# Optimization experiments

Hardware: AMD Instinct MI355X
Metric: run time of the kernel (lower is better)

The kernel has to match this reference:

```python
import jax, jax.numpy as jnp
import numpy as np

B, N, C = 4, 48 * 64, 256
H, W = 48, 64


def _positional_encodings(batch, dtype=jnp.float32):
    # (x^2, y^2, xy, x, y, 1) encoding; matches get_positional_encodings with intrinsics=None
    ys = jnp.linspace(-1.0, 1.0, H, dtype=dtype)
    xs = jnp.linspace(-1.0, 1.0, W, dtype=dtype)
    p3 = jnp.tile(ys, W)            # [N] : ys repeated W times (torch .repeat(B, w))
    p4 = jnp.repeat(xs, H)          # [N] : each x repeated H times (repeat_interleave)
    pos = jnp.stack([p3 * p3, p4 * p4, p3 * p4, p3, p4, jnp.ones_like(p3)], axis=-1)  # [N,6]
    return jnp.broadcast_to(pos, (batch, N, 6))


def setup_inputs() -> dict:
    key = jax.random.key(0)
    k1, k2, k3, k4 = jax.random.split(key, 4)
    x1 = jax.random.normal(k1, (B, N, C), dtype=jnp.float32)
    x2 = jax.random.normal(k2, (B, N, C), dtype=jnp.float32)
    corr = jax.random.normal(k3, (B, 1, H, W, H, W), dtype=jnp.float32)
    W_proj = jax.random.normal(k4, (C + 6, C), dtype=jnp.float32) * (1.0 / np.sqrt(C + 6))
    b_proj = jnp.zeros((C,), dtype=jnp.float32)
    return {"x1": x1, "x2": x2, "corr": corr, "W_proj": W_proj, "b_proj": b_proj}


def reference(x1, x2, corr, W_proj, b_proj):
    b, n, c = x1.shape
    a = corr.reshape(b, n, n)                      # squeeze(1) + double flatten
    # dual softmax (row-wise * column-wise)
    s_row = jax.nn.softmax(a, axis=-1)
    s_col = jax.nn.softmax(a, axis=-2)
    attn_f1 = s_row * s_col                        # [B,N,N]
    attn_f2 = jnp.swapaxes(attn_f1, -2, -1)        # softmax(a^T,-1)*softmax(a^T,-2) == attn_f1^T

    pos = _positional_encodings(b, dtype=x1.dtype)
    v1 = jnp.concatenate([x1, pos], axis=2)        # [B,N,C+6]
    v2 = jnp.concatenate([x2, pos], axis=2)

    # bilinear products v^T @ attn @ v  -> [B, C+6, C+6]
    fund1 = jnp.einsum('bnc,bnm,bmd->bcd', v1, attn_f1, v1)
    fund2 = jnp.einsum('bnc,bnm,bmd->bcd', v2, attn_f2, v2)

    fund1 = jnp.swapaxes(fund1, -2, -1)
    fund2 = jnp.swapaxes(fund2, -2, -1)

    out1 = fund1 @ W_proj + b_proj                 # proj_fundamental
    out2 = fund2 @ W_proj + b_proj
    return (out2, out1)                            # (fundamental_2, fundamental_1)
```

## Files before the change

### kernel.cpp

```cpp
#include <hip/hip_runtime.h>
#include <math.h>

#define NB 4
#define NN 3072
#define NC 256
#define CP 262
#define KG 384
#define XW 528
#define MD 272
#define K3S 8
#define HH 48
#define WW 64
#define LOG2E 1.4426950408889634f

typedef short short8 __attribute__((ext_vector_type(8)));
typedef short short4v __attribute__((ext_vector_type(4)));
typedef float f32x4 __attribute__((ext_vector_type(4)));
typedef unsigned int uint4v __attribute__((ext_vector_type(4)));

__device__ __forceinline__ float fexp2(float x) {
#if __has_builtin(__builtin_amdgcn_exp2f)
    return __builtin_amdgcn_exp2f(x);
#else
    return __exp2f(x);
#endif
}

__device__ __forceinline__ void bsplit(float v, short& h, short& l) {
    unsigned u = __float_as_uint(v);
    h = (short)(u >> 16);
    float r = v - __uint_as_float(u & 0xFFFF0000u);
    l = (short)(__float_as_uint(r) >> 16);
}

__device__ __forceinline__ void fma4(float4& c, float a, float4 b) {
    c.x = fmaf(a, b.x, c.x);
    c.y = fmaf(a, b.y, c.y);
    c.z = fmaf(a, b.z, c.z);
    c.w = fmaf(a, b.w, c.w);
}

__global__ __launch_bounds__(256) void k_prep(const float* __restrict__ x1,
                                              const float* __restrict__ x2,
                                              short* __restrict__ Xh, short* __restrict__ Xl) {
    int id = blockIdx.x * 256 + threadIdx.x;
    if (id >= NB * KG * XW) return;
    int col = id % XW;
    int rest = id / XW;
    int kg = rest % KG;
    int b = rest / KG;
    short* ph = Xh + (size_t)id * 8;
    short* pl = Xl + (size_t)id * 8;
    if (col < 512) {
        const float* src = (col < 256 ? x1 : x2) + ((size_t)b * NN + kg * 8) * NC + (col & 255);
#pragma unroll
        for (int j = 0; j < 8; j++) {
            short hs, ls;
            bsplit(src[(size_t)j * NC], hs, ls);
            ph[j] = hs; pl[j] = ls;
        }
    } else {
        int c = col - 512;
#pragma unroll
        for (int j = 0; j < 8; j++) {
            int k = kg * 8 + j;
            int ip4 = k / HH;
            int ip3 = k - ip4 * HH;
            float p3 = -1.f + 2.f * (float)ip3 / 47.f;
            float p4 = -1.f + 2.f * (float)ip4 / 63.f;
            float v = 0.f;
            if (c == 0) v = p3 * p3;
            else if (c == 1) v = p4 * p4;
            else if (c == 2) v = p3 * p4;
            else if (c == 3) v = p3;
            else if (c == 4) v = p4;
            else if (c == 5) v = 1.f;
            short hs, ls;
            bsplit(v, hs, ls);
            ph[j] = hs; pl[j] = ls;
        }
    }
}

__global__ __launch_bounds__(256) void k_stats(const float* __restrict__ corr,
                                               float* __restrict__ pM, float* __restrict__ pS,
                                               float* __restrict__ rmS, float* __restrict__ irs) {
    int bid = blockIdx.x;
    int t = threadIdx.x;
    __shared__ float red[8];
    if (bid < 384) {
        int cx = bid % 12;
        int b = (bid / 12) & 3;
        int ch = bid / 48;
        int m = cx * 256 + t;
        const float* p = corr + (size_t)b * NN * NN + (size_t)ch * 384 * NN + m;
        float mx[4], s[4];
#pragma unroll
        for (int i = 0; i < 4; i++) { mx[i] = -3.4e38f; s[i] = 0.f; }
        for (int r = 0; r < 384; r += 4) {
#pragma unroll
            for (int i = 0; i < 4; i++) {
                float x = p[(size_t)(r + i) * NN];
                float mn = fmaxf(mx[i], x);
                s[i] = s[i] * __expf(mx[i] - mn) + __expf(x - mn);
                mx[i] = mn;
            }
        }
        float mn01 = fmaxf(mx[0], mx[1]);
        float s01 = s[0] * __expf(mx[0] - mn01) + s[1] * __expf(mx[1] - mn01);
        float mn23 = fmaxf(mx[2], mx[3]);
        float s23 = s[2] * __expf(mx[2] - mn23) + s[3] * __expf(mx[3] - mn23);
        float mnA = fmaxf(mn01, mn23);
        float sA = s01 * __expf(mn01 - mnA) + s23 * __expf(mn23 - mnA);
        pM[((size_t)ch * NB + b) * NN + m] = mnA;
        pS[((size_t)ch * NB + b) * NN + m] = sA;
    } else {
        int rid = bid - 384;
        int b = rid / NN;
        int n = rid - b * NN;
        const float4* p = (const float4*)(corr + ((size_t)b * NN + n) * NN);
        float4 v[3];
        float m = -3.4e38f;
#pragma unroll
        for (int i = 0; i < 3; i++) {
            v[i] = p[t + i * 256];
            m = fmaxf(m, fmaxf(fmaxf(v[i].x, v[i].y), fmaxf(v[i].z, v[i].w)));
        }
#pragma unroll
        for (int off = 32; off; off >>= 1) m = fmaxf(m, __shfl_xor(m, off));
        if ((t & 63) == 0) red[t >> 6] = m;
        __syncthreads();
        m = fmaxf(fmaxf(red[0], red[1]), fmaxf(red[2], red[3]));
        float s = 0.f;
#pragma unroll
        for (int i = 0; i < 3; i++)
            s += __expf(v[i].x - m) + __expf(v[i].y - m) + __expf(v[i].z - m) + __expf(v[i].w - m);
#pragma unroll
        for (int off = 32; off; off >>= 1) s += __shfl_xor(s, off);
        if ((t & 63) == 0) red[4 + (t >> 6)] = s;
        __syncthreads();
        if (t == 0) {
            float st = red[4] + red[5] + red[6] + red[7];
            rmS[b * NN + n] = m * LOG2E;
            irs[b * NN + n] = 1.f / st;
        }
    }
}

__global__ __launch_bounds__(256) void k_colcombine(const float* __restrict__ pM,
                                                    const float* __restrict__ pS,
                                                    float* __restrict__ ccS) {
    int idx = blockIdx.x * 256 + threadIdx.x;
    if (idx >= NB * NN) return;
    float mx = -3.4e38f, s = 0.f;
#pragma unroll
    for (int ch = 0; ch < 8; ch++) {
        float m2 = pM[(size_t)ch * NB * NN + idx];
        float s2 = pS[(size_t)ch * NB * NN + idx];
        float mn = fmaxf(mx, m2);
        s = s * __expf(mx - mn) + s2 * __expf(m2 - mn);
        mx = mn;
    }
    ccS[idx] = (mx + logf(s)) * LOG2E;
}

#define MFMA_CLUSTER(AHF, ALF, BHF, BLF)                                                          \
    {                                                                                             \
        _Pragma("unroll") for (int fr_ = 0; fr_ < 3; fr_++)                                       \
        _Pragma("unroll") for (int i_ = 0; i_ < 4; i_++)                                          \
            acc[fr_][i_] = __builtin_amdgcn_mfma_f32_16x16x32_bf16(AHF[fr_], BHF[i_], acc[fr_][i_], 0, 0, 0); \
        _Pragma("unroll") for (int fr_ = 0; fr_ < 3; fr_++)                                       \
        _Pragma("unroll") for (int i_ = 0; i_ < 4; i_++)                                          \
            acc[fr_][i_] = __builtin_amdgcn_mfma_f32_16x16x32_bf16(AHF[fr_], BLF[i_], acc[fr_][i_], 0, 0, 0); \
        _Pragma("unroll") for (int fr_ = 0; fr_ < 3; fr_++)                                       \
        _Pragma("unroll") for (int i_ = 0; i_ < 4; i_++)                                          \
            acc[fr_][i_] = __builtin_amdgcn_mfma_f32_16x16x32_bf16(ALF[fr_], BHF[i_], acc[fr_][i_], 0, 0, 0); \
    }

#define POS_CLUSTER(AHF, ALF, PBH, PBL)                                                           \
    {                                                                                             \
        _Pragma("unroll") for (int fr_ = 0; fr_ < 3; fr_++) {                                     \
            accP[fr_] = __builtin_amdgcn_mfma_f32_16x16x32_bf16(AHF[fr_], (PBH), accP[fr_], 0, 0, 0); \
            accP[fr_] = __builtin_amdgcn_mfma_f32_16x16x32_bf16(AHF[fr_], (PBL), accP[fr_], 0, 0, 0); \
            accP[fr_] = __builtin_amdgcn_mfma_f32_16x16x32_bf16(ALF[fr_], (PBH), accP[fr_], 0, 0, 0); \
        }                                                                                         \
    }

#define READ_AFRAGS(BUFH, BUFL, UNIT, AHF, ALF)                                                   \
    {                                                                                             \
        _Pragma("unroll") for (int fr_ = 0; fr_ < 3; fr_++) {                                     \
            int rowr_ = rbase + fr_ * 16 + row16;                                                 \
            int uidx_ = rowr_ * 32 + (((UNIT) ^ (rowr_ & 7)) << 2);                               \
            AHF[fr_] = *(const short8*)&(BUFH)[uidx_];                                            \
            ALF[fr_] = *(const short8*)&(BUFL)[uidx_];                                            \
        }                                                                                         \
    }

#define LOAD_B(PH, PL, BHF, BLF)                                                                  \
    {                                                                                             \
        _Pragma("unroll") for (int i_ = 0; i_ < 4; i_++) {                                        \
            BHF[i_] = *(const short8*)((PH) + i_ * 128);                                          \
            BLF[i_] = *(const short8*)((PL) + i_ * 128);                                          \
        }                                                                                         \
    }

#define STAGE_A(DSTH, DSTL, PC)                                                                   \
    {                                                                                             \
        f32x4 ccv0 = *(const f32x4*)&ccsh[(PC) * 64 + g * 16];                                    \
        f32x4 ccv1 = *(const f32x4*)&ccsh[(PC) * 64 + g * 16 + 4];                                \
        f32x4 ccv2 = *(const f32x4*)&ccsh[(PC) * 64 + g * 16 + 8];                                \
        f32x4 ccv3 = *(const f32x4*)&ccsh[(PC) * 64 + g * 16 + 12];                               \
        float ev[16];                                                                             \
        _Pragma("unroll") for (int q_ = 0; q_ < 4; q_++) {                                        \
            ev[q_]      = fexp2(fmaf(C2, cr[0][q_], rmn) - ccv0[q_]);                             \
            ev[4 + q_]  = fexp2(fmaf(C2, cr[1][q_], rmn) - ccv1[q_]);                             \
            ev[8 + q_]  = fexp2(fmaf(C2, cr[2][q_], rmn) - ccv2[q_]);                             \
            ev[12 + q_] = fexp2(fmaf(C2, cr[3][q_], rmn) - ccv3[q_]);                             \
        }                                                                                         \
        uint4v hi0, hi1, lo0, lo1;                                                                \
        _Pragma("unroll") for (int q_ = 0; q_ < 4; q_++) {                                        \
            unsigned u0 = __float_as_uint(ev[2 * q_]);                                            \
            unsigned u1 = __float_as_uint(ev[2 * q_ + 1]);                                        \
            hi0[q_] = __builtin_amdgcn_perm(u1, u0, 0x07060302u);                                 \
            float r0_ = ev[2 * q_] - __uint_as_float(u0 & 0xffff0000u);                           \
            float r1_ = ev[2 * q_ + 1] - __uint_as_float(u1 & 0xffff0000u);                       \
            lo0[q_] = __builtin_amdgcn_perm(__float_as_uint(r1_), __float_as_uint(r0_), 0x07060302u); \
            unsigned v0 = __float_as_uint(ev[8 + 2 * q_]);                                        \
            unsigned v1 = __float_as_uint(ev[8 + 2 * q_ + 1]);                                    \
            hi1[q_] = __builtin_amdgcn_perm(v1, v0, 0x07060302u);                                 \
            float t0_ = ev[8 + 2 * q_] - __uint_as_float(v0 & 0xffff0000u);                       \
            float t1_ = ev[8 + 2 * q_ + 1] - __uint_as_float(v1 & 0xffff0000u);                   \
            lo1[q_] = __builtin_amdgcn_perm(__float_as_uint(t1_), __float_as_uint(t0_), 0x07060302u); \
        }                                                                                         \
        *(uint4v*)&(DSTH)[widx0] = hi0;                                                           \
        *(uint4v*)&(DSTH)[widx1] = hi1;                                                           \
        *(uint4v*)&(DSTL)[widx0] = lo0;                                                           \
        *(uint4v*)&(DSTL)[widx1] = lo1;                                                           \
    }

__global__ __launch_bounds__(512, 2) void k2_mfma(const float* __restrict__ corr,
        const short* __restrict__ Xh, const short* __restrict__ Xl,
        const float* __restrict__ rmS, const float* __restrict__ irs,
        const float* __restrict__ ccS,
        short* __restrict__ Zh, short* __restrict__ Zl) {
    __shared__ __align__(16) unsigned AHs[2][96 * 32];
    __shared__ __align__(16) unsigned ALs[2][96 * 32];
    __shared__ __align__(16) float ccsh[NN];

    const float C2 = 2.f * LOG2E;
    const size_t BSTEP = (size_t)4 * XW * 8;

    int bid = blockIdx.x;
    int xcd = bid & 7, sub = bid >> 3;
    int b = xcd >> 1;
    int which = sub & 1;
    int rowblk = (xcd & 1) + ((sub >> 1) << 1);
    int n0 = rowblk * 96;

    int t = threadIdx.x;
    int w = t >> 6, l = t & 63;
    int row16 = l & 15, slot = l >> 4;
    int rg = w & 1, cg = w >> 1;
    int rbase = rg * 48;
    bool posw = (which == 0) && (cg == 3);
    bool writer = (t < 384);
    int wrow = t >> 2, g = t & 3;
    int widx0 = wrow * 32 + (((2 * g) ^ (wrow & 7)) << 2);
    int widx1 = wrow * 32 + (((2 * g + 1) ^ (wrow & 7)) << 2);

    {
        const f32x4* src = (const f32x4*)(ccS + (size_t)b * NN);
        for (int i = t; i < NN / 4; i += 512) ((f32x4*)ccsh)[i] = src[i];
    }

    const float* corrR = corr;
    float rmn = 0.f;
    if (writer) {
        corrR = corr + ((size_t)b * NN + n0 + wrow) * NN + g * 16;
        rmn = -rmS[b * NN + n0 + wrow];
    }

    int col0 = which * 256 + cg * 64 + row16;
    const short* bh = Xh + ((size_t)(b * KG + slot) * XW + col0) * 8;
    const short* bl = Xl + ((size_t)(b * KG + slot) * XW + col0) * 8;
    const short* ph = Xh + ((size_t)(b * KG + slot) * XW + 512 + row16) * 8;
    const short* plp = Xl + ((size_t)(b * KG + slot) * XW + 512 + row16) * 8;

    f32x4 acc[3][4];
    f32x4 accP[3];
    const f32x4 zz = {0.f, 0.f, 0.f, 0.f};
#pragma unroll
    for (int fr = 0; fr < 3; fr++) {
#pragma unroll
        for (int i = 0; i < 4; i++) acc[fr][i] = zz;
        accP[fr] = zz;
    }

    short8 BhA[4], BlA[4], BhB[4], BlB[4];
    short8 PbhA = {0,0,0,0,0,0,0,0}, PblA = PbhA, PbhB = PbhA, PblB = PbhA;
    LOAD_B(bh, bl, BhA, BlA);
    if (posw) { PbhA = *(const short8*)ph; PblA = *(const short8*)plp; }

    f32x4 cr[4];
    __syncthreads();
    if (writer) {
#pragma unroll
        for (int q = 0; q < 4; q++) cr[q] = *(const f32x4*)(corrR + q * 4);
        STAGE_A(AHs[0], ALs[0], 0);
#pragma unroll
        for (int q = 0; q < 4; q++) cr[q] = *(const f32x4*)(corrR + 64 + q * 4);
    }
    asm volatile("s_waitcnt lgkmcnt(0)" ::: "memory");
    __builtin_amdgcn_s_barrier();

    int cur = 0;
    for (int p = 0; p < 48; ++p) {
        const unsigned* AHc = &AHs[cur][0];
        const unsigned* ALc = &ALs[cur][0];
        unsigned* AHn = &AHs[cur ^ 1][0];
        unsigned* ALn = &ALs[cur ^ 1][0];
        short8 Ah[3], Al[3];
        READ_AFRAGS(AHc, ALc, slot, Ah, Al);
        bh += BSTEP; bl += BSTEP;
        LOAD_B(bh, bl, BhB, BlB);
        if (posw) { ph += BSTEP; plp += BSTEP; PbhB = *(const short8*)ph; PblB = *(const short8*)plp; }
        MFMA_CLUSTER(Ah, Al, BhA, BlA);
        if (posw) POS_CLUSTER(Ah, Al, PbhA, PblA);
        READ_AFRAGS(AHc, ALc, 4 + slot, Ah, Al);
        if (p < 47) {
            bh += BSTEP; bl += BSTEP;
            LOAD_B(bh, bl, BhA, BlA);
            if (posw) { ph += BSTEP; plp += BSTEP; PbhA = *(const short8*)ph; PblA = *(const short8*)plp; }
        }
        if (writer) {
            int pc = (p + 1 < 48) ? p + 1 : 47;
            STAGE_A(AHn, ALn, pc);
            int pn = (p + 2 < 48) ? p + 2 : 47;
#pragma unroll
            for (int q = 0; q < 4; q++) cr[q] = *(const f32x4*)(corrR + pn * 64 + q * 4);
        }
        MFMA_CLUSTER(Ah, Al, BhB, BlB);
        if (posw) POS_CLUSTER(Ah, Al, PbhB, PblB);
        asm volatile("s_waitcnt lgkmcnt(0)" ::: "memory");
        __builtin_amdgcn_s_barrier();
        cur ^= 1;
    }

#pragma unroll
    for (int fr = 0; fr < 3; fr++) {
        f32x4 sv = *(const f32x4*)(irs + b * NN + n0 + rbase + fr * 16 + slot * 4);
        int kgz = rowblk * 12 + rg * 6 + fr * 2 + (slot >> 1);
        int jb = (slot & 1) << 2;
#pragma unroll
        for (int i = 0; i < 4; i++) {
            int colv = which * 256 + cg * 64 + i * 16 + row16;
            size_t off = ((size_t)(b * KG + kgz) * XW + colv) * 8 + jb;
            short4v zh, zl;
#pragma unroll
            for (int r = 0; r < 4; r++) {
                float vv = acc[fr][i][r] * sv[r];
                short hs, ls; bsplit(vv, hs, ls);
                zh[r] = hs; zl[r] = ls;
            }
            *(short4v*)(Zh + off) = zh;
            *(short4v*)(Zl + off) = zl;
        }
        if (posw && cg == 3 && rg == (w & 1)) {  }
        if (posw) {
            size_t off = ((size_t)(b * KG + kgz) * XW + 512 + row16) * 8 + jb;
            short4v zh, zl;
#pragma unroll
            for (int r = 0; r < 4; r++) {
                float vv = accP[fr][r] * sv[r];
                short hs, ls; bsplit(vv, hs, ls);
                zh[r] = hs; zl[r] = ls;
            }
            *(short4v*)(Zh + off) = zh;
            *(short4v*)(Zl + off) = zl;
        }
    }
}

__global__ __launch_bounds__(256) void k3_mfma(const short* __restrict__ Xh, const short* __restrict__ Xl,
                                               const short* __restrict__ Zh, const short* __restrict__ Zl,
                                               float* __restrict__ Mpart) {
    int tile = blockIdx.x;
    int rt = tile / 3, ct = tile % 3;
    int mb = blockIdx.y;
    int mat = mb >> 2, b = mb & 3;
    int split = blockIdx.z;

    const int O0[4] = {0, 6, 12, 17};
    int r0f = O0[rt], rNf = O0[rt + 1] - r0f;
    int c0f = O0[ct], cNf = O0[ct + 1] - c0f;

    int t = threadIdx.x;
    int w = t >> 6, l = t & 63;
    int row16 = l & 15, slot = l >> 4;
    int wr = w >> 1, wc = w & 1;
    int rh = (rNf + 1) >> 1;
    int rbeg = r0f + (wr ? rh : 0);
    int rcnt = wr ? (rNf - rh) : rh;
    int chh = (cNf + 1) >> 1;
    int cbeg = c0f + (wc ? chh : 0);
    int ccnt = wc ? (cNf - chh) : chh;

    const short *Ah_, *Al_, *Bh_, *Bl_;
    int abase, bbase;
    if (mat == 0) { Ah_ = Xh; Al_ = Xl; Bh_ = Zh; Bl_ = Zl; abase = 0; bbase = 0; }
    else          { Ah_ = Zh; Al_ = Zl; Bh_ = Xh; Bl_ = Xl; abase = 256; bbase = 256; }

    int acol[3], bcol[3];
#pragma unroll
    for (int i = 0; i < 3; i++) {
        int fa = rbeg + i;
        acol[i] = ((fa < 16) ? (abase + fa * 16) : 512) + row16;
        int fb = cbeg + i;
        bcol[i] = ((fb < 16) ? (bbase + fb * 16) : 512) + row16;
    }

    f32x4 acc[3][3];
    const f32x4 zz = {0.f, 0.f, 0.f, 0.f};
#pragma unroll
    for (int i = 0; i < 3; i++)
#pragma unroll
        for (int j = 0; j < 3; j++) acc[i][j] = zz;

    for (int it = 0; it < 12; it++) {
        int kg = split * 48 + it * 4 + slot;
        size_t base = (size_t)(b * KG + kg) * XW;
        short8 Ah[3], Al[3], Bhf[3], Blf[3];
#pragma unroll
        for (int i = 0; i < 3; i++) {
            if (i < rcnt) {
                Ah[i] = *(const short8*)(Ah_ + (base + acol[i]) * 8);
                Al[i] = *(const short8*)(Al_ + (base + acol[i]) * 8);
            }
            if (i < ccnt) {
                Bhf[i] = *(const short8*)(Bh_ + (base + bcol[i]) * 8);
                Blf[i] = *(const short8*)(Bl_ + (base + bcol[i]) * 8);
            }
        }
#pragma unroll
        for (int i = 0; i < 3; i++) {
            if (i < rcnt) {
#pragma unroll
                for (int j = 0; j < 3; j++) {
                    if (j < ccnt) {
                        acc[i][j] = __builtin_amdgcn_mfma_f32_16x16x32_bf16(Ah[i], Bhf[j], acc[i][j], 0, 0, 0);
                        acc[i][j] = __builtin_amdgcn_mfma_f32_16x16x32_bf16(Al[i], Bhf[j], acc[i][j], 0, 0, 0);
                        acc[i][j] = __builtin_amdgcn_mfma_f32_16x16x32_bf16(Ah[i], Blf[j], acc[i][j], 0, 0, 0);
                    }
                }
            }
        }
    }

    float* Mp = Mpart + (size_t)(mb * K3S + split) * (MD * MD);
#pragma unroll
    for (int i = 0; i < 3; i++) {
        if (i < rcnt) {
#pragma unroll
            for (int j = 0; j < 3; j++) {
                if (j < ccnt) {
                    int r = (rbeg + i) * 16 + slot * 4;
                    int c = (cbeg + j) * 16 + row16;
#pragma unroll
                    for (int q = 0; q < 4; q++)
                        Mp[(size_t)(r + q) * MD + c] = acc[i][j][q];
                }
            }
        }
    }
}

__global__ __launch_bounds__(256) void k_mcombine(const float* __restrict__ Mpart, float* __restrict__ M) {
    const int per = MD * MD;
    int f4 = blockIdx.x * 256 + threadIdx.x;
    if (f4 >= (8 * per) / 4) return;
    int e = f4 * 4;
    int mb = e / per;
    int off = e - mb * per;
    const float* src = Mpart + (size_t)mb * K3S * per + off;
    float4 s = make_float4(0.f, 0.f, 0.f, 0.f);
#pragma unroll
    for (int sp = 0; sp < K3S; sp++) {
        float4 v = *(const float4*)(src + (size_t)sp * per);
        s.x += v.x; s.y += v.y; s.z += v.z; s.w += v.w;
    }
    *(float4*)(M + (size_t)mb * per + off) = s;
}

__global__ __launch_bounds__(256) void k4_proj(const float* __restrict__ M, const float* __restrict__ Wp,
                                               const float* __restrict__ bp, float* __restrict__ out) {
    int i0 = blockIdx.x * 16;
    int b = blockIdx.y;
    int mat = blockIdx.z;
    const float* Mp = M + (size_t)(mat * 4 + b) * (MD * MD);
    int t = threadIdx.x;
    int jt = t & 63, it = t >> 6;
    int j = jt * 4;
    float4 a0 = make_float4(0.f, 0.f, 0.f, 0.f), a1 = a0, a2 = a0, a3 = a0;
#pragma unroll 2
    for (int k = 0; k < CP; k++) {
        float4 w = *(const float4*)(Wp + (size_t)k * NC + j);
        float4 g = *(const float4*)(Mp + (size_t)k * MD + i0 + it * 4);
        fma4(a0, g.x, w); fma4(a1, g.y, w); fma4(a2, g.z, w); fma4(a3, g.w, w);
    }
    float4 bb = *(const float4*)(bp + j);
    a0.x += bb.x; a0.y += bb.y; a0.z += bb.z; a0.w += bb.w;
    a1.x += bb.x; a1.y += bb.y; a1.z += bb.z; a1.w += bb.w;
    a2.x += bb.x; a2.y += bb.y; a2.z += bb.z; a2.w += bb.w;
    a3.x += bb.x; a3.y += bb.y; a3.z += bb.z; a3.w += bb.w;
    float* ob = out + (mat == 0 ? (size_t)NB * CP * NC : (size_t)0) + (size_t)b * CP * NC;
    int i = i0 + it * 4;
    if (i + 0 < CP) *(float4*)(ob + (size_t)(i + 0) * NC + j) = a0;
    if (i + 1 < CP) *(float4*)(ob + (size_t)(i + 1) * NC + j) = a1;
    if (i + 2 < CP) *(float4*)(ob + (size_t)(i + 2) * NC + j) = a2;
    if (i + 3 < CP) *(float4*)(ob + (size_t)(i + 3) * NC + j) = a3;
}

extern "C" void kernel_launch(void* const* d_in, const int* in_sizes, int n_in,
                              void* d_out, int out_size, void* d_ws, size_t ws_size,
                              hipStream_t stream) {
    const float* x1 = (const float*)d_in[0];
    const float* x2 = (const float*)d_in[1];
    const float* corr = (const float*)d_in[2];
    const float* Wp = (const float*)d_in[3];
    const float* bp = (const float*)d_in[4];
    float* out = (float*)d_out;
    float* w = (float*)d_ws;

    const size_t XSZ = (size_t)NB * KG * XW * 8;

    size_t o = 0;
    float* rmS = w + o;   o += NB * NN;
    float* irs = w + o;   o += NB * NN;
    float* ccS = w + o;   o += NB * NN;
    float* pM = w + o;    o += 8 * NB * NN;
    float* pS = w + o;    o += 8 * NB * NN;
    short* Xh = (short*)(w + o); o += XSZ / 2;
    short* Xl = (short*)(w + o); o += XSZ / 2;
    short* Zh = (short*)(w + o); o += XSZ / 2;
    short* Zl = (short*)(w + o); o += XSZ / 2;
    float* Mpart = w + o; o += (size_t)8 * K3S * MD * MD;
    float* M = w + o;     o += (size_t)8 * MD * MD;

    k_prep<<<dim3(3168), dim3(256), 0, stream>>>(x1, x2, Xh, Xl);
    k_stats<<<dim3(384 + NB * NN), dim3(256), 0, stream>>>(corr, pM, pS, rmS, irs);
    k_colcombine<<<dim3(48), dim3(256), 0, stream>>>(pM, pS, ccS);
    k2_mfma<<<dim3(256), dim3(512), 0, stream>>>(corr, Xh, Xl, rmS, irs, ccS, Zh, Zl);
    k3_mfma<<<dim3(9, 8, K3S), dim3(256), 0, stream>>>(Xh, Xl, Zh, Zl, Mpart);
    k_mcombine<<<dim3(578), dim3(256), 0, stream>>>(Mpart, M);
    k4_proj<<<dim3(17, NB, 2), dim3(256), 0, stream>>>(M, Wp, bp, out);
}
```

Measured before the change: 248.1 us.

## Fuse prep/colcombine/mcombine into neighbors and retile k2 warps over rows

Merges the bf16 split prep work into the stats kernel, moves the column-softmax combine into k2's prologue, and folds the K-split partial reduction into the projection kernel. This drops three launches and their intermediate buffers. Row stats now use one wave per row instead of a block-level reduction with barriers. In k2, each warp now covers all 96 rows and 32 columns, and the positional-encoding MFMA work rotates across warps with a shared-memory reduction at the end. The costs are redundant combine work per k2 block, eight-fold partial reads per k-step in the projection, and a larger A-fragment register footprint.

```diff
diff --git a/kernel.cpp b/kernel.cpp
--- a/kernel.cpp
+++ b/kernel.cpp
@@ -40,54 +40,14 @@
     c.w = fmaf(a, b.w, c.w);
 }
 
-__global__ __launch_bounds__(256) void k_prep(const float* __restrict__ x1,
-                                              const float* __restrict__ x2,
-                                              short* __restrict__ Xh, short* __restrict__ Xl) {
-    int id = blockIdx.x * 256 + threadIdx.x;
-    if (id >= NB * KG * XW) return;
-    int col = id % XW;
-    int rest = id / XW;
-    int kg = rest % KG;
-    int b = rest / KG;
-    short* ph = Xh + (size_t)id * 8;
-    short* pl = Xl + (size_t)id * 8;
-    if (col < 512) {
-        const float* src = (col < 256 ? x1 : x2) + ((size_t)b * NN + kg * 8) * NC + (col & 255);
-#pragma unroll
-        for (int j = 0; j < 8; j++) {
-            short hs, ls;
-            bsplit(src[(size_t)j * NC], hs, ls);
-            ph[j] = hs; pl[j] = ls;
-        }
-    } else {
-        int c = col - 512;
-#pragma unroll
-        for (int j = 0; j < 8; j++) {
-            int k = kg * 8 + j;
-            int ip4 = k / HH;
-            int ip3 = k - ip4 * HH;
-            float p3 = -1.f + 2.f * (float)ip3 / 47.f;
-            float p4 = -1.f + 2.f * (float)ip4 / 63.f;
-            float v = 0.f;
-            if (c == 0) v = p3 * p3;
-            else if (c == 1) v = p4 * p4;
-            else if (c == 2) v = p3 * p4;
-            else if (c == 3) v = p3;
-            else if (c == 4) v = p4;
-            else if (c == 5) v = 1.f;
-            short hs, ls;
-            bsplit(v, hs, ls);
-            ph[j] = hs; pl[j] = ls;
-        }
-    }
-}
-
 __global__ __launch_bounds__(256) void k_stats(const float* __restrict__ corr,
+                                               const float* __restrict__ x1,
+                                               const float* __restrict__ x2,
                                                float* __restrict__ pM, float* __restrict__ pS,
-                                               float* __restrict__ rmS, float* __restrict__ irs) {
+                                               float* __restrict__ rmS, float* __restrict__ irs,
+                                               short* __restrict__ Xh, short* __restrict__ Xl) {
     int bid = blockIdx.x;
     int t = threadIdx.x;
-    __shared__ float red[8];
     if (bid < 384) {
         int cx = bid % 12;
         int b = (bid / 12) & 3;
@@ -114,94 +74,120 @@
         float sA = s01 * __expf(mn01 - mnA) + s23 * __expf(mn23 - mnA);
         pM[((size_t)ch * NB + b) * NN + m] = mnA;
         pS[((size_t)ch * NB + b) * NN + m] = sA;
+    } else if (bid < 3456) {
+        int rid = bid - 384;
+        int b = rid / 768;
+        int r0 = (rid - b * 768) * 4;
+        int w = t >> 6, l = t & 63;
+        int n = r0 + w;
+        const float4* p = (const float4*)(corr + ((size_t)b * NN + n) * NN);
+        float4 v[12];
+        float m = -3.4e38f;
+#pragma unroll
+        for (int i = 0; i < 12; i++) {
+            v[i] = p[l + i * 64];
+            m = fmaxf(m, fmaxf(fmaxf(v[i].x, v[i].y), fmaxf(v[i].z, v[i].w)));
+        }
+#pragma unroll
+        for (int off = 1; off < 64; off <<= 1) m = fmaxf(m, __shfl_xor(m, off));
+        float s = 0.f;
+#pragma unroll
+        for (int i = 0; i < 12; i++)
+            s += __expf(v[i].x - m) + __expf(v[i].y - m) + __expf(v[i].z - m) + __expf(v[i].w - m);
+#pragma unroll
+        for (int off = 1; off < 64; off <<= 1) s += __shfl_xor(s, off);
+        if (l == 0) {
+            rmS[b * NN + n] = m * LOG2E;
+            irs[b * NN + n] = 1.f / s;
+        }
     } else {
-        int rid = bid - 384;
-        int b = rid / NN;
-        int n = rid - b * NN;
-        const float4* p = (const float4*)(corr + ((size_t)b * NN + n) * NN);
-        float4 v[3];
-        float m = -3.4e38f;
-#pragma unroll
-        for (int i = 0; i < 3; i++) {
-            v[i] = p[t + i * 256];
-            m = fmaxf(m, fmaxf(fmaxf(v[i].x, v[i].y), fmaxf(v[i].z, v[i].w)));
-        }
-#pragma unroll
-        for (int off = 32; off; off >>= 1) m = fmaxf(m, __shfl_xor(m, off));
-        if ((t & 63) == 0) red[t >> 6] = m;
-        __syncthreads();
-        m = fmaxf(fmaxf(red[0], red[1]), fmaxf(red[2], red[3]));
-        float s = 0.f;
-#pragma unroll
-        for (int i = 0; i < 3; i++)
-            s += __expf(v[i].x - m) + __expf(v[i].y - m) + __expf(v[i].z - m) + __expf(v[i].w - m);
-#pragma unroll
-        for (int off = 32; off; off >>= 1) s += __shfl_xor(s, off);
-        if ((t & 63) == 0) red[4 + (t >> 6)] = s;
-        __syncthreads();
-        if (t == 0) {
-            float st = red[4] + red[5] + red[6] + red[7];
-            rmS[b * NN + n] = m * LOG2E;
-            irs[b * NN + n] = 1.f / st;
-        }
-    }
-}
-
-__global__ __launch_bounds__(256) void k_colcombine(const float* __restrict__ pM,
-                                                    const float* __restrict__ pS,
-                                                    float* __restrict__ ccS) {
-    int idx = blockIdx.x * 256 + threadIdx.x;
-    if (idx >= NB * NN) return;
-    float mx = -3.4e38f, s = 0.f;
-#pragma unroll
-    for (int ch = 0; ch < 8; ch++) {
-        float m2 = pM[(size_t)ch * NB * NN + idx];
-        float s2 = pS[(size_t)ch * NB * NN + idx];
-        float mn = fmaxf(mx, m2);
-        s = s * __expf(mx - mn) + s2 * __expf(m2 - mn);
-        mx = mn;
-    }
-    ccS[idx] = (mx + logf(s)) * LOG2E;
-}
-
-#define MFMA_CLUSTER(AHF, ALF, BHF, BLF)                                                          \
-    {                                                                                             \
-        _Pragma("unroll") for (int fr_ = 0; fr_ < 3; fr_++)                                       \
-        _Pragma("unroll") for (int i_ = 0; i_ < 4; i_++)                                          \
+        int id = (bid - 3456) * 256 + t;
+        int col = id % XW;
+        int rest = id / XW;
+        int kg = rest % KG;
+        int b = rest / KG;
+        short* ph = Xh + (size_t)id * 8;
+        short* pl = Xl + (size_t)id * 8;
+        if (col < 512) {
+            const float* src = (col < 256 ? x1 : x2) + ((size_t)b * NN + kg * 8) * NC + (col & 255);
+#pragma unroll
+            for (int j = 0; j < 8; j++) {
+                short hs, ls;
+                bsplit(src[(size_t)j * NC], hs, ls);
+                ph[j] = hs; pl[j] = ls;
+            }
+        } else {
+            int c = col - 512;
+#pragma unroll
+            for (int j = 0; j < 8; j++) {
+                int k = kg * 8 + j;
+                int ip4 = k / HH;
+                int ip3 = k - ip4 * HH;
+                float p3 = -1.f + 2.f * (float)ip3 / 47.f;
+                float p4 = -1.f + 2.f * (float)ip4 / 63.f;
+                float v = 0.f;
+                if (c == 0) v = p3 * p3;
+                else if (c == 1) v = p4 * p4;
+                else if (c == 2) v = p3 * p4;
+                else if (c == 3) v = p3;
+                else if (c == 4) v = p4;
+                else if (c == 5) v = 1.f;
+                short hs, ls;
+                bsplit(v, hs, ls);
+                ph[j] = hs; pl[j] = ls;
+            }
+        }
+    }
+}
+
+struct SMemMain {
+    unsigned AH[2][96 * 32];
+    unsigned AL[2][96 * 32];
+    float ccsh[NN];
+};
+union SMemU {
+    SMemMain m;
+    float pdump[8 * 64 * 24];
+};
+
+#define LOAD_B2(PH, PL, BHF, BLF)                                           \
+    {                                                                        \
+        BHF[0] = *(const short8*)(PH);                                       \
+        BHF[1] = *(const short8*)((PH) + 128);                               \
+        BLF[0] = *(const short8*)(PL);                                       \
+        BLF[1] = *(const short8*)((PL) + 128);                               \
+    }
+
+#define READ_AFRAGS6(BUFH, BUFL, UNIT, AHF, ALF)                             \
+    {                                                                        \
+        _Pragma("unroll") for (int fr_ = 0; fr_ < 6; fr_++) {                \
+            int rowr_ = fr_ * 16 + row16;                                    \
+            int uidx_ = rowr_ * 32 + (((UNIT) ^ (rowr_ & 7)) << 2);          \
+            AHF[fr_] = *(const short8*)&(BUFH)[uidx_];                       \
+            ALF[fr_] = *(const short8*)&(BUFL)[uidx_];                       \
+        }                                                                    \
+    }
+
+#define MFMA_CLUSTER62(AHF, ALF, BHF, BLF)                                                         \
+    {                                                                                              \
+        _Pragma("unroll") for (int fr_ = 0; fr_ < 6; fr_++)                                        \
+        _Pragma("unroll") for (int i_ = 0; i_ < 2; i_++)                                           \
             acc[fr_][i_] = __builtin_amdgcn_mfma_f32_16x16x32_bf16(AHF[fr_], BHF[i_], acc[fr_][i_], 0, 0, 0); \
-        _Pragma("unroll") for (int fr_ = 0; fr_ < 3; fr_++)                                       \
-        _Pragma("unroll") for (int i_ = 0; i_ < 4; i_++)                                          \
+        _Pragma("unroll") for (int fr_ = 0; fr_ < 6; fr_++)                                        \
+        _Pragma("unroll") for (int i_ = 0; i_ < 2; i_++)                                           \
             acc[fr_][i_] = __builtin_amdgcn_mfma_f32_16x16x32_bf16(AHF[fr_], BLF[i_], acc[fr_][i_], 0, 0, 0); \
-        _Pragma("unroll") for (int fr_ = 0; fr_ < 3; fr_++)                                       \
-        _Pragma("unroll") for (int i_ = 0; i_ < 4; i_++)                                          \
+        _Pragma("unroll") for (int fr_ = 0; fr_ < 6; fr_++)                                        \
+        _Pragma("unroll") for (int i_ = 0; i_ < 2; i_++)                                           \
             acc[fr_][i_] = __builtin_amdgcn_mfma_f32_16x16x32_bf16(ALF[fr_], BHF[i_], acc[fr_][i_], 0, 0, 0); \
     }
 
-#define POS_CLUSTER(AHF, ALF, PBH, PBL)                                                           \
-    {                                                                                             \
-        _Pragma("unroll") for (int fr_ = 0; fr_ < 3; fr_++) {                                     \
+#define POS_CLUSTER6(AHF, ALF, PBH, PBL)                                                           \
+    {                                                                                              \
+        _Pragma("unroll") for (int fr_ = 0; fr_ < 6; fr_++) {                                      \
             accP[fr_] = __builtin_amdgcn_mfma_f32_16x16x32_bf16(AHF[fr_], (PBH), accP[fr_], 0, 0, 0); \
             accP[fr_] = __builtin_amdgcn_mfma_f32_16x16x32_bf16(AHF[fr_], (PBL), accP[fr_], 0, 0, 0); \
             accP[fr_] = __builtin_amdgcn_mfma_f32_16x16x32_bf16(ALF[fr_], (PBH), accP[fr_], 0, 0, 0); \
-        }                                                                                         \
-    }
-
-#define READ_AFRAGS(BUFH, BUFL, UNIT, AHF, ALF)                                                   \
-    {                                                                                             \
-        _Pragma("unroll") for (int fr_ = 0; fr_ < 3; fr_++) {                                     \
-            int rowr_ = rbase + fr_ * 16 + row16;                                                 \
-            int uidx_ = rowr_ * 32 + (((UNIT) ^ (rowr_ & 7)) << 2);                               \
-            AHF[fr_] = *(const short8*)&(BUFH)[uidx_];                                            \
-            ALF[fr_] = *(const short8*)&(BUFL)[uidx_];                                            \
-        }                                                                                         \
-    }
-
-#define LOAD_B(PH, PL, BHF, BLF)                                                                  \
-    {                                                                                             \
-        _Pragma("unroll") for (int i_ = 0; i_ < 4; i_++) {                                        \
-            BHF[i_] = *(const short8*)((PH) + i_ * 128);                                          \
-            BLF[i_] = *(const short8*)((PL) + i_ * 128);                                          \
-        }                                                                                         \
+        }                                                                                          \
     }
 
 #define STAGE_A(DSTH, DSTL, PC)                                                                   \
@@ -241,11 +227,10 @@
 __global__ __launch_bounds__(512, 2) void k2_mfma(const float* __restrict__ corr,
         const short* __restrict__ Xh, const short* __restrict__ Xl,
         const float* __restrict__ rmS, const float* __restrict__ irs,
-        const float* __restrict__ ccS,
+        const float* __restrict__ pM, const float* __restrict__ pS,
         short* __restrict__ Zh, short* __restrict__ Zl) {
-    __shared__ __align__(16) unsigned AHs[2][96 * 32];
-    __shared__ __align__(16) unsigned ALs[2][96 * 32];
-    __shared__ __align__(16) float ccsh[NN];
+    __shared__ SMemU sm;
+    float* ccsh = sm.m.ccsh;
 
     const float C2 = 2.f * LOG2E;
     const size_t BSTEP = (size_t)4 * XW * 8;
@@ -260,17 +245,23 @@
     int t = threadIdx.x;
     int w = t >> 6, l = t & 63;
     int row16 = l & 15, slot = l >> 4;
-    int rg = w & 1, cg = w >> 1;
-    int rbase = rg * 48;
-    bool posw = (which == 0) && (cg == 3);
+    bool doPos = (which == 0);
     bool writer = (t < 384);
     int wrow = t >> 2, g = t & 3;
     int widx0 = wrow * 32 + (((2 * g) ^ (wrow & 7)) << 2);
     int widx1 = wrow * 32 + (((2 * g + 1) ^ (wrow & 7)) << 2);
 
-    {
-        const f32x4* src = (const f32x4*)(ccS + (size_t)b * NN);
-        for (int i = t; i < NN / 4; i += 512) ((f32x4*)ccsh)[i] = src[i];
+    for (int c = t; c < NN; c += 512) {
+        float mx = -3.4e38f, s = 0.f;
+#pragma unroll
+        for (int ch = 0; ch < 8; ch++) {
+            float m2 = pM[(size_t)ch * NB * NN + b * NN + c];
+            float s2 = pS[(size_t)ch * NB * NN + b * NN + c];
+            float mn = fmaxf(mx, m2);
+            s = s * __expf(mx - mn) + s2 * __expf(m2 - mn);
+            mx = mn;
+        }
+        ccsh[c] = fmaf(mx, LOG2E, __log2f(s));
     }
 
     const float* corrR = corr;
@@ -280,33 +271,28 @@
         rmn = -rmS[b * NN + n0 + wrow];
     }
 
-    int col0 = which * 256 + cg * 64 + row16;
+    int col0 = which * 256 + w * 32 + row16;
     const short* bh = Xh + ((size_t)(b * KG + slot) * XW + col0) * 8;
     const short* bl = Xl + ((size_t)(b * KG + slot) * XW + col0) * 8;
-    const short* ph = Xh + ((size_t)(b * KG + slot) * XW + 512 + row16) * 8;
-    const short* plp = Xl + ((size_t)(b * KG + slot) * XW + 512 + row16) * 8;
-
-    f32x4 acc[3][4];
-    f32x4 accP[3];
+
+    f32x4 acc[6][2];
+    f32x4 accP[6];
     const f32x4 zz = {0.f, 0.f, 0.f, 0.f};
 #pragma unroll
-    for (int fr = 0; fr < 3; fr++) {
-#pragma unroll
-        for (int i = 0; i < 4; i++) acc[fr][i] = zz;
-        accP[fr] = zz;
-    }
-
-    short8 BhA[4], BlA[4], BhB[4], BlB[4];
-    short8 PbhA = {0,0,0,0,0,0,0,0}, PblA = PbhA, PbhB = PbhA, PblB = PbhA;
-    LOAD_B(bh, bl, BhA, BlA);
-    if (posw) { PbhA = *(const short8*)ph; PblA = *(const short8*)plp; }
+    for (int fr = 0; fr < 6; fr++) {
+        acc[fr][0] = zz; acc[fr][1] = zz; accP[fr] = zz;
+    }
+
+    short8 BhA[2], BlA[2], BhB[2], BlB[2];
+    short8 P0h = {0,0,0,0,0,0,0,0}, P0l = P0h, P1h = P0h, P1l = P0h;
+    LOAD_B2(bh, bl, BhA, BlA);
 
     f32x4 cr[4];
     __syncthreads();
     if (writer) {
 #pragma unroll
         for (int q = 0; q < 4; q++) cr[q] = *(const f32x4*)(corrR + q * 4);
-        STAGE_A(AHs[0], ALs[0], 0);
+        STAGE_A(sm.m.AH[0], sm.m.AL[0], 0);
 #pragma unroll
         for (int q = 0; q < 4; q++) cr[q] = *(const f32x4*)(corrR + 64 + q * 4);
     }
@@ -315,22 +301,28 @@
 
     int cur = 0;
     for (int p = 0; p < 48; ++p) {
-        const unsigned* AHc = &AHs[cur][0];
-        const unsigned* ALc = &ALs[cur][0];
-        unsigned* AHn = &AHs[cur ^ 1][0];
-        unsigned* ALn = &ALs[cur ^ 1][0];
-        short8 Ah[3], Al[3];
-        READ_AFRAGS(AHc, ALc, slot, Ah, Al);
+        const unsigned* AHc = &sm.m.AH[cur][0];
+        const unsigned* ALc = &sm.m.AL[cur][0];
+        unsigned* AHn = &sm.m.AH[cur ^ 1][0];
+        unsigned* ALn = &sm.m.AL[cur ^ 1][0];
+        bool duty = doPos && (w == (p & 7));
+        if (duty) {
+            size_t o0 = ((size_t)(b * KG + p * 8 + slot) * XW + 512 + row16) * 8;
+            P0h = *(const short8*)(Xh + o0);
+            P0l = *(const short8*)(Xl + o0);
+            P1h = *(const short8*)(Xh + o0 + BSTEP);
+            P1l = *(const short8*)(Xl + o0 + BSTEP);
+        }
+        short8 Ah[6], Al[6];
+        READ_AFRAGS6(AHc, ALc, slot, Ah, Al);
         bh += BSTEP; bl += BSTEP;
-        LOAD_B(bh, bl, BhB, BlB);
-        if (posw) { ph += BSTEP; plp += BSTEP; PbhB = *(const short8*)ph; PblB = *(const short8*)plp; }
-        MFMA_CLUSTER(Ah, Al, BhA, BlA);
-        if (posw) POS_CLUSTER(Ah, Al, PbhA, PblA);
-        READ_AFRAGS(AHc, ALc, 4 + slot, Ah, Al);
+        LOAD_B2(bh, bl, BhB, BlB);
+        MFMA_CLUSTER62(Ah, Al, BhA, BlA);
+        if (duty) POS_CLUSTER6(Ah, Al, P0h, P0l);
+        READ_AFRAGS6(AHc, ALc, 4 + slot, Ah, Al);
         if (p < 47) {
             bh += BSTEP; bl += BSTEP;
-            LOAD_B(bh, bl, BhA, BlA);
-            if (posw) { ph += BSTEP; plp += BSTEP; PbhA = *(const short8*)ph; PblA = *(const short8*)plp; }
+            LOAD_B2(bh, bl, BhA, BlA);
         }
         if (writer) {
             int pc = (p + 1 < 48) ? p + 1 : 47;
@@ -339,21 +331,21 @@
 #pragma unroll
             for (int q = 0; q < 4; q++) cr[q] = *(const f32x4*)(corrR + pn * 64 + q * 4);
         }
-        MFMA_CLUSTER(Ah, Al, BhB, BlB);
-        if (posw) POS_CLUSTER(Ah, Al, PbhB, PblB);
+        MFMA_CLUSTER62(Ah, Al, BhB, BlB);
+        if (duty) POS_CLUSTER6(Ah, Al, P1h, P1l);
         asm volatile("s_waitcnt lgkmcnt(0)" ::: "memory");
         __builtin_amdgcn_s_barrier();
         cur ^= 1;
     }
 
 #pragma unroll
-    for (int fr = 0; fr < 3; fr++) {
-        f32x4 sv = *(const f32x4*)(irs + b * NN + n0 + rbase + fr * 16 + slot * 4);
-        int kgz = rowblk * 12 + rg * 6 + fr * 2 + (slot >> 1);
+    for (int fr = 0; fr < 6; fr++) {
+        f32x4 sv = *(const f32x4*)(irs + b * NN + n0 + fr * 16 + slot * 4);
+        int kgz = rowblk * 12 + fr * 2 + (slot >> 1);
         int jb = (slot & 1) << 2;
 #pragma unroll
-        for (int i = 0; i < 4; i++) {
-            int colv = which * 256 + cg * 64 + i * 16 + row16;
+        for (int i = 0; i < 2; i++) {
+            int colv = which * 256 + w * 32 + i * 16 + row16;
             size_t off = ((size_t)(b * KG + kgz) * XW + colv) * 8 + jb;
             short4v zh, zl;
 #pragma unroll
@@ -365,19 +357,33 @@
             *(short4v*)(Zh + off) = zh;
             *(short4v*)(Zl + off) = zl;
         }
-        if (posw && cg == 3 && rg == (w & 1)) {  }
-        if (posw) {
-            size_t off = ((size_t)(b * KG + kgz) * XW + 512 + row16) * 8 + jb;
-            short4v zh, zl;
-#pragma unroll
-            for (int r = 0; r < 4; r++) {
-                float vv = accP[fr][r] * sv[r];
-                short hs, ls; bsplit(vv, hs, ls);
-                zh[r] = hs; zl[r] = ls;
-            }
-            *(short4v*)(Zh + off) = zh;
-            *(short4v*)(Zl + off) = zl;
-        }
+    }
+    if (doPos) {
+#pragma unroll
+        for (int fr = 0; fr < 6; fr++)
+            *(f32x4*)&sm.pdump[(size_t)(w * 64 + l) * 24 + fr * 4] = accP[fr];
+    }
+    __syncthreads();
+    if (doPos && t < 384) {
+        int fr = t >> 6, ll = t & 63;
+        int sl = ll >> 4, r16 = ll & 15;
+        f32x4 s = zz;
+#pragma unroll
+        for (int ww = 0; ww < 8; ww++)
+            s += *(const f32x4*)&sm.pdump[(size_t)(ww * 64 + ll) * 24 + fr * 4];
+        f32x4 sv = *(const f32x4*)(irs + b * NN + n0 + fr * 16 + sl * 4);
+        int kgz = rowblk * 12 + fr * 2 + (sl >> 1);
+        int jb = (sl & 1) << 2;
+        size_t off = ((size_t)(b * KG + kgz) * XW + 512 + r16) * 8 + jb;
+        short4v zh, zl;
+#pragma unroll
+        for (int r = 0; r < 4; r++) {
+            float vv = s[r] * sv[r];
+            short hs, ls; bsplit(vv, hs, ls);
+            zh[r] = hs; zl[r] = ls;
+        }
+        *(short4v*)(Zh + off) = zh;
+        *(short4v*)(Zl + off) = zl;
     }
 }
 
@@ -474,38 +480,25 @@
     }
 }
 
-__global__ __launch_bounds__(256) void k_mcombine(const float* __restrict__ Mpart, float* __restrict__ M) {
-    const int per = MD * MD;
-    int f4 = blockIdx.x * 256 + threadIdx.x;
-    if (f4 >= (8 * per) / 4) return;
-    int e = f4 * 4;
-    int mb = e / per;
-    int off = e - mb * per;
-    const float* src = Mpart + (size_t)mb * K3S * per + off;
-    float4 s = make_float4(0.f, 0.f, 0.f, 0.f);
-#pragma unroll
-    for (int sp = 0; sp < K3S; sp++) {
-        float4 v = *(const float4*)(src + (size_t)sp * per);
-        s.x += v.x; s.y += v.y; s.z += v.z; s.w += v.w;
-    }
-    *(float4*)(M + (size_t)mb * per + off) = s;
-}
-
-__global__ __launch_bounds__(256) void k4_proj(const float* __restrict__ M, const float* __restrict__ Wp,
+__global__ __launch_bounds__(256) void k4_proj(const float* __restrict__ Mpart, const float* __restrict__ Wp,
                                                const float* __restrict__ bp, float* __restrict__ out) {
     int i0 = blockIdx.x * 16;
     int b = blockIdx.y;
     int mat = blockIdx.z;
-    const float* Mp = M + (size_t)(mat * 4 + b) * (MD * MD);
+    const float* Mp = Mpart + (size_t)((mat * 4 + b) * K3S) * (MD * MD);
     int t = threadIdx.x;
     int jt = t & 63, it = t >> 6;
     int j = jt * 4;
     float4 a0 = make_float4(0.f, 0.f, 0.f, 0.f), a1 = a0, a2 = a0, a3 = a0;
-#pragma unroll 2
     for (int k = 0; k < CP; k++) {
         float4 w = *(const float4*)(Wp + (size_t)k * NC + j);
-        float4 g = *(const float4*)(Mp + (size_t)k * MD + i0 + it * 4);
-        fma4(a0, g.x, w); fma4(a1, g.y, w); fma4(a2, g.z, w); fma4(a3, g.w, w);
+        float4 gsum = make_float4(0.f, 0.f, 0.f, 0.f);
+#pragma unroll
+        for (int sp = 0; sp < K3S; sp++) {
+            float4 gv = *(const float4*)(Mp + (size_t)sp * MD * MD + (size_t)k * MD + i0 + it * 4);
+            gsum.x += gv.x; gsum.y += gv.y; gsum.z += gv.z; gsum.w += gv.w;
+        }
+        fma4(a0, gsum.x, w); fma4(a1, gsum.y, w); fma4(a2, gsum.z, w); fma4(a3, gsum.w, w);
     }
     float4 bb = *(const float4*)(bp + j);
     a0.x += bb.x; a0.y += bb.y; a0.z += bb.z; a0.w += bb.w;
@@ -536,7 +529,6 @@
     size_t o = 0;
     float* rmS = w + o;   o += NB * NN;
     float* irs = w + o;   o += NB * NN;
-    float* ccS = w + o;   o += NB * NN;
     float* pM = w + o;    o += 8 * NB * NN;
     float* pS = w + o;    o += 8 * NB * NN;
     short* Xh = (short*)(w + o); o += XSZ / 2;
@@ -544,13 +536,9 @@
     short* Zh = (short*)(w + o); o += XSZ / 2;
     short* Zl = (short*)(w + o); o += XSZ / 2;
     float* Mpart = w + o; o += (size_t)8 * K3S * MD * MD;
-    float* M = w + o;     o += (size_t)8 * MD * MD;
-
-    k_prep<<<dim3(3168), dim3(256), 0, stream>>>(x1, x2, Xh, Xl);
-    k_stats<<<dim3(384 + NB * NN), dim3(256), 0, stream>>>(corr, pM, pS, rmS, irs);
-    k_colcombine<<<dim3(48), dim3(256), 0, stream>>>(pM, pS, ccS);
-    k2_mfma<<<dim3(256), dim3(512), 0, stream>>>(corr, Xh, Xl, rmS, irs, ccS, Zh, Zl);
+
+    k_stats<<<dim3(6624), dim3(256), 0, stream>>>(corr, x1, x2, pM, pS, rmS, irs, Xh, Xl);
+    k2_mfma<<<dim3(256), dim3(512), 0, stream>>>(corr, Xh, Xl, rmS, irs, pM, pS, Zh, Zl);
     k3_mfma<<<dim3(9, 8, K3S), dim3(256), 0, stream>>>(Xh, Xl, Zh, Zl, Mpart);
-    k_mcombine<<<dim3(578), dim3(256), 0, stream>>>(Mpart, M);
-    k4_proj<<<dim3(17, NB, 2), dim3(256), 0, stream>>>(M, Wp, bp, out);
-}
+    k4_proj<<<dim3(17, NB, 2), dim3(256), 0, stream>>>(Mpart, Wp, bp, out);
+}
```

Result: slower. 362.3 us (+46.0%).
